# Performance work log

Hardware: AMD Instinct MI355X
Metric: run time of the kernel (lower is better)

The kernel has to match this reference:

```python
import jax, jax.numpy as jnp
import numpy as np

PATCH_SIZE = 9
EPS = 1e-05


def to_patches(x, p):
    # x: [b, c, H, W] -> [b, c*(H-p+1)*(W-p+1), p, p]
    # matches torch unfold(2,p,1).unfold(3,p,1) + rearrange 'b c p1 p2 h w -> b (c p1 p2) h w'
    b, c, H, W = x.shape
    Hp, Wp = H - p + 1, W - p + 1
    # fixed small loop over p*p offsets (p=9); XLA fuses these slices
    pat = jnp.stack([x[:, :, i:i + Hp, j:j + Wp] for i in range(p) for j in range(p)], axis=2)
    pat = pat.reshape(b, c, p, p, Hp, Wp)
    pat = jnp.transpose(pat, (0, 1, 4, 5, 2, 3))  # b c Hp Wp p p
    return pat.reshape(b, c * Hp * Wp, p, p)


def _norm(x, eps):
    # per-channel normalization over last two dims (population variance, correction=0)
    mu = jnp.mean(x, axis=(-1, -2), keepdims=True)
    var = jnp.mean((x - mu) ** 2, axis=(-1, -2), keepdims=True) + eps
    return (x - mu) / jnp.sqrt(var)


def setup_inputs() -> dict:
    key = jax.random.key(0)
    k1, k2, k3 = jax.random.split(key, 3)
    b, c, H, W, p = 8, 1, 128, 128, PATCH_SIZE
    Hp, Wp = H - p + 1, W - p + 1
    x1 = jax.random.normal(k1, (b, c, H, W), dtype=jnp.float32)
    x2 = jax.random.normal(k2, (b, c, H, W), dtype=jnp.float32)
    mask2 = jax.random.uniform(k3, (b, c * Hp * Wp, p, p), dtype=jnp.float32)
    return {"x1": x1, "x2": x2, "mask2": mask2}


def reference(x1, x2, mask2):
    p = PATCH_SIZE
    x1p = to_patches(x1, p)
    x2p = to_patches(x2, p)
    _, c, h, w = x1p.shape
    x2p = x2p * mask2
    x1n = _norm(x1p, EPS)
    x2n = _norm(x2p, EPS)
    score = jnp.einsum('bchw,bchw->b', x1n, x2n)
    return score / (c * h * w)
```

## Files before the change

### kernel.cpp

```cpp
#include <hip/hip_runtime.h>


#define BATCH 8
#define HH    128
#define WW    128
#define PP    9
#define HP    120
#define WP    120
#define NPATCH (HP * WP)
#define PSQ   (PP * PP)
#define EPSF  1e-5f

__device__ __forceinline__ void gload16(const void* g, void* lds) {
    __builtin_amdgcn_global_load_lds(
        (const __attribute__((address_space(1))) void*)g,
        (__attribute__((address_space(3))) void*)lds, 16, 0, 0);
}

__global__ __launch_bounds__(256) void ncc_kernel(const float* __restrict__ x1,
                                                  const float* __restrict__ x2,
                                                  const float* __restrict__ mask,
                                                  float* __restrict__ part)
{
    const int blk  = blockIdx.x;
    const int b    = blk / HP;
    const int i    = blk - b * HP;
    const int tid  = threadIdx.x;
    const int lane = tid & 63;

    __shared__ __align__(16) float m_lds[WP * PSQ];
    __shared__ __align__(16) float x1_lds[PP * WW];
    __shared__ __align__(16) float x2_lds[PP * WW];
    __shared__ float wsum[4];

    {
        const float4* msrc = reinterpret_cast<const float4*>(
            mask + ((size_t)b * NPATCH + (size_t)i * WP) * PSQ);
        char* mdst = reinterpret_cast<char*>(m_lds);
        #pragma unroll
        for (int k = 0; k < 10; ++k) {
            int g = k * 256 + tid;
            if (g < (WP * PSQ) / 4)
                gload16(msrc + g, mdst + (size_t)(g - lane) * 16);
        }
    }
    {
        const float4* s1 = reinterpret_cast<const float4*>(x1 + ((size_t)b * HH + i) * WW);
        const float4* s2 = reinterpret_cast<const float4*>(x2 + ((size_t)b * HH + i) * WW);
        char* d1 = reinterpret_cast<char*>(x1_lds);
        char* d2 = reinterpret_cast<char*>(x2_lds);
        #pragma unroll
        for (int k = 0; k < 2; ++k) {
            int g = k * 256 + tid;
            if (g < (PP * WW) / 4) {
                gload16(s1 + g, d1 + (size_t)(g - lane) * 16);
                gload16(s2 + g, d2 + (size_t)(g - lane) * 16);
            }
        }
    }
    __syncthreads();

    float val = 0.0f;
    const int j = tid >> 1;
    const int h = tid & 1;
    if (j < WP) {
        const int r0 = h ? 5 : 0;
        const int r1 = h ? 9 : 5;
        float sa = 0.f, saa = 0.f, sb = 0.f, sbb = 0.f, sab = 0.f;
        const float* mp = m_lds + j * PSQ + r0 * PP;
        for (int r = r0; r < r1; ++r) {
            const float* x1r = x1_lds + r * WW + j;
            const float* x2r = x2_lds + r * WW + j;
            #pragma unroll
            for (int cc = 0; cc < PP; ++cc) {
                float a  = x1r[cc];
                float bv = x2r[cc] * mp[cc];
                sa += a;
                saa = fmaf(a, a, saa);
                sb += bv;
                sbb = fmaf(bv, bv, sbb);
                sab = fmaf(a, bv, sab);
            }
            mp += PP;
        }
        sa  += __shfl_xor(sa, 1);
        saa += __shfl_xor(saa, 1);
        sb  += __shfl_xor(sb, 1);
        sbb += __shfl_xor(sbb, 1);
        sab += __shfl_xor(sab, 1);
        if (h == 0) {
            const float invN = 1.0f / 81.0f;
            float mua  = sa * invN;
            float mub  = sb * invN;
            float vara = saa * invN - mua * mua + EPSF;
            float varb = sbb * invN - mub * mub + EPSF;
            float cov  = sab - 81.0f * mua * mub;
            val = cov / sqrtf(vara * varb);
        }
    }

    #pragma unroll
    for (int off = 32; off > 0; off >>= 1)
        val += __shfl_down(val, off);
    const int wave = tid >> 6;
    if ((tid & 63) == 0) wsum[wave] = val;
    __syncthreads();
    if (tid == 0)
        part[blk] = wsum[0] + wsum[1] + wsum[2] + wsum[3];
}

__global__ __launch_bounds__(128) void finalize_kernel(const float* __restrict__ part,
                                                       float* __restrict__ out)
{
    const int b = blockIdx.x;
    const int t = threadIdx.x;
    float v = (t < HP) ? part[b * HP + t] : 0.0f;
    #pragma unroll
    for (int off = 32; off > 0; off >>= 1)
        v += __shfl_down(v, off);
    __shared__ float s[2];
    if ((t & 63) == 0) s[t >> 6] = v;
    __syncthreads();
    if (t == 0)
        out[b] = (s[0] + s[1]) * (1.0f / ((float)NPATCH * (float)PSQ));
}

extern "C" void kernel_launch(void* const* d_in, const int* in_sizes, int n_in,
                              void* d_out, int out_size, void* d_ws, size_t ws_size,
                              hipStream_t stream) {
    const float* x1   = (const float*)d_in[0];
    const float* x2   = (const float*)d_in[1];
    const float* mask = (const float*)d_in[2];
    float* out  = (float*)d_out;
    float* part = (float*)d_ws;

    ncc_kernel<<<BATCH * HP, 256, 0, stream>>>(x1, x2, mask, part);
    finalize_kernel<<<BATCH, 128, 0, stream>>>(part, out);
}
```

Measured before the change: 17.18 us.

## Split each output row across two blocks of half-width columns

Each block now handles 60 patch columns of one row instead of 120, doubling the grid to 1920 blocks of 128 threads. The image tile staged in LDS shrinks to a 72-column window and the mask slab halves. The intent is to expose more blocks so more CUs are busy and LDS per block drops, which raises occupancy for this memory-bound kernel. The cost is some redundant image-row loads for the overlapping halo and twice as many partial sums for the finalize kernel to reduce.

```diff
diff --git a/kernel.cpp b/kernel.cpp
--- a/kernel.cpp
+++ b/kernel.cpp
@@ -10,6 +10,9 @@
 #define NPATCH (HP * WP)
 #define PSQ   (PP * PP)
 #define EPSF  1e-5f
+#define CP    60
+#define XW    72
+#define NBLK  (BATCH * HP * 2)
 
 __device__ __forceinline__ void gload16(const void* g, void* lds) {
     __builtin_amdgcn_global_load_lds(
@@ -17,44 +20,49 @@
         (__attribute__((address_space(3))) void*)lds, 16, 0, 0);
 }
 
-__global__ __launch_bounds__(256) void ncc_kernel(const float* __restrict__ x1,
+__global__ __launch_bounds__(128) void ncc_kernel(const float* __restrict__ x1,
                                                   const float* __restrict__ x2,
                                                   const float* __restrict__ mask,
                                                   float* __restrict__ part)
 {
     const int blk  = blockIdx.x;
-    const int b    = blk / HP;
-    const int i    = blk - b * HP;
+    const int b    = blk / 240;
+    const int rest = blk - b * 240;
+    const int i    = rest >> 1;
+    const int j0   = (rest & 1) * CP;
     const int tid  = threadIdx.x;
     const int lane = tid & 63;
 
-    __shared__ __align__(16) float m_lds[WP * PSQ];
-    __shared__ __align__(16) float x1_lds[PP * WW];
-    __shared__ __align__(16) float x2_lds[PP * WW];
-    __shared__ float wsum[4];
+    __shared__ __align__(16) float m_lds[CP * PSQ];
+    __shared__ __align__(16) float x_lds[2][PP][XW];
+    __shared__ float wsum[2];
 
     {
         const float4* msrc = reinterpret_cast<const float4*>(
-            mask + ((size_t)b * NPATCH + (size_t)i * WP) * PSQ);
+            mask + ((size_t)b * NPATCH + (size_t)i * WP + j0) * PSQ);
         char* mdst = reinterpret_cast<char*>(m_lds);
         #pragma unroll
         for (int k = 0; k < 10; ++k) {
-            int g = k * 256 + tid;
-            if (g < (WP * PSQ) / 4)
+            int g = k * 128 + tid;
+            if (g < (CP * PSQ) / 4)
                 gload16(msrc + g, mdst + (size_t)(g - lane) * 16);
         }
     }
     {
-        const float4* s1 = reinterpret_cast<const float4*>(x1 + ((size_t)b * HH + i) * WW);
-        const float4* s2 = reinterpret_cast<const float4*>(x2 + ((size_t)b * HH + i) * WW);
-        char* d1 = reinterpret_cast<char*>(x1_lds);
-        char* d2 = reinterpret_cast<char*>(x2_lds);
+        const float4* s1 = reinterpret_cast<const float4*>(
+            x1 + ((size_t)(b * HH + i)) * WW + j0);
+        const float4* s2 = reinterpret_cast<const float4*>(
+            x2 + ((size_t)(b * HH + i)) * WW + j0);
+        char* d1 = reinterpret_cast<char*>(&x_lds[0][0][0]);
+        char* d2 = reinterpret_cast<char*>(&x_lds[1][0][0]);
         #pragma unroll
         for (int k = 0; k < 2; ++k) {
-            int g = k * 256 + tid;
-            if (g < (PP * WW) / 4) {
-                gload16(s1 + g, d1 + (size_t)(g - lane) * 16);
-                gload16(s2 + g, d2 + (size_t)(g - lane) * 16);
+            int t = k * 128 + tid;
+            if (t < (PP * XW) / 4) {
+                int r  = t / (XW / 4);
+                int c4 = t - r * (XW / 4);
+                gload16(s1 + r * (WW / 4) + c4, d1 + (size_t)(t - lane) * 16);
+                gload16(s2 + r * (WW / 4) + c4, d2 + (size_t)(t - lane) * 16);
             }
         }
     }
@@ -63,14 +71,14 @@
     float val = 0.0f;
     const int j = tid >> 1;
     const int h = tid & 1;
-    if (j < WP) {
+    if (j < CP) {
         const int r0 = h ? 5 : 0;
         const int r1 = h ? 9 : 5;
         float sa = 0.f, saa = 0.f, sb = 0.f, sbb = 0.f, sab = 0.f;
-        const float* mp = m_lds + j * PSQ + r0 * PP;
+        const float* mp = m_lds + j * PSQ + h * 45;
         for (int r = r0; r < r1; ++r) {
-            const float* x1r = x1_lds + r * WW + j;
-            const float* x2r = x2_lds + r * WW + j;
+            const float* x1r = &x_lds[0][r][j];
+            const float* x2r = &x_lds[1][r][j];
             #pragma unroll
             for (int cc = 0; cc < PP; ++cc) {
                 float a  = x1r[cc];
@@ -102,27 +110,26 @@
     #pragma unroll
     for (int off = 32; off > 0; off >>= 1)
         val += __shfl_down(val, off);
-    const int wave = tid >> 6;
-    if ((tid & 63) == 0) wsum[wave] = val;
+    if ((tid & 63) == 0) wsum[tid >> 6] = val;
     __syncthreads();
     if (tid == 0)
-        part[blk] = wsum[0] + wsum[1] + wsum[2] + wsum[3];
+        part[blk] = wsum[0] + wsum[1];
 }
 
-__global__ __launch_bounds__(128) void finalize_kernel(const float* __restrict__ part,
+__global__ __launch_bounds__(256) void finalize_kernel(const float* __restrict__ part,
                                                        float* __restrict__ out)
 {
     const int b = blockIdx.x;
     const int t = threadIdx.x;
-    float v = (t < HP) ? part[b * HP + t] : 0.0f;
+    float v = (t < 240) ? part[b * 240 + t] : 0.0f;
     #pragma unroll
     for (int off = 32; off > 0; off >>= 1)
         v += __shfl_down(v, off);
-    __shared__ float s[2];
+    __shared__ float s[4];
     if ((t & 63) == 0) s[t >> 6] = v;
     __syncthreads();
     if (t == 0)
-        out[b] = (s[0] + s[1]) * (1.0f / ((float)NPATCH * (float)PSQ));
+        out[b] = (s[0] + s[1] + s[2] + s[3]) * (1.0f / ((float)NPATCH * (float)PSQ));
 }
 
 extern "C" void kernel_launch(void* const* d_in, const int* in_sizes, int n_in,
@@ -134,6 +141,6 @@
     float* out  = (float*)d_out;
     float* part = (float*)d_ws;
 
-    ncc_kernel<<<BATCH * HP, 256, 0, stream>>>(x1, x2, mask, part);
-    finalize_kernel<<<BATCH, 128, 0, stream>>>(part, out);
+    ncc_kernel<<<NBLK, 128, 0, stream>>>(x1, x2, mask, part);
+    finalize_kernel<<<BATCH, 256, 0, stream>>>(part, out);
 }
```

Result: slower. 17.56 us (+2.2%).
